# Performance work log

Hardware: AMD Instinct MI355X
Metric: run time of the kernel (lower is better)

The kernel has to match this reference:

```python
import jax, jax.numpy as jnp
import numpy as np

DEPTH = 2
TWO_PI = 6.283185307179586


def _apply_ry(state, theta, axis):
    """Apply RY(theta) on qubit at `axis` of state [N,2,2,2,2]. theta: [N] or scalar."""
    half = theta * 0.5
    a0 = jnp.take(state, 0, axis=axis)  # [N,2,2,2]
    a1 = jnp.take(state, 1, axis=axis)
    c = jnp.reshape(jnp.cos(half), (-1,) + (1,) * (a0.ndim - 1))
    s = jnp.reshape(jnp.sin(half), (-1,) + (1,) * (a0.ndim - 1))
    return jnp.stack([c * a0 - s * a1, s * a0 + c * a1], axis=axis)


def _apply_cnot(state, c_axis, t_axis):
    a0 = jnp.take(state, 0, axis=c_axis)  # control=0: unchanged
    a1 = jnp.take(state, 1, axis=c_axis)  # control=1: flip target
    t_ax = t_axis - (1 if t_axis > c_axis else 0)
    a1 = jnp.flip(a1, axis=t_ax)
    return jnp.stack([a0, a1], axis=c_axis)


def _simulate(patches, weights):
    """patches: [N,4] angles. Returns <Z_i> for i=0..3, shape [N,4]. All gates real."""
    N = patches.shape[0]
    state = jnp.zeros((N, 2, 2, 2, 2), dtype=patches.dtype)
    state = state.at[:, 0, 0, 0, 0].set(1.0)
    for w in range(4):  # data encoding
        state = _apply_ry(state, patches[:, w], axis=w + 1)
    for d in range(DEPTH):  # variational layers
        for w in range(4):
            state = _apply_ry(state, weights[d, w], axis=w + 1)
        for c, t in ((0, 1), (1, 2), (2, 3)):
            state = _apply_cnot(state, c + 1, t + 1)
    probs = state * state
    zs = []
    for w in range(4):
        p0 = jnp.take(probs, 0, axis=w + 1).sum(axis=(1, 2, 3))
        p1 = jnp.take(probs, 1, axis=w + 1).sum(axis=(1, 2, 3))
        zs.append(p0 - p1)
    return jnp.stack(zs, axis=-1)  # [N,4]


def setup_inputs() -> dict:
    key = jax.random.key(0)
    k1, k2, k3, k4 = jax.random.split(key, 4)
    B = 8192
    x = jax.random.uniform(k1, (B, 1, 28, 28), dtype=jnp.float32)
    weights = jax.random.uniform(k2, (DEPTH, 4), dtype=jnp.float32) * TWO_PI
    W = jax.random.normal(k3, (10, 4 * 14 * 14), dtype=jnp.float32) * 0.02
    b = jax.random.normal(k4, (10,), dtype=jnp.float32) * 0.02
    return {"x": x, "weights": weights, "W": W, "b": b}


def reference(x, weights, W, b):
    B = x.shape[0]
    # Extract non-overlapping 2x2 patches in row-major (i,j) order;
    # within a patch, order is [(i,j),(i,j+1),(i+1,j),(i+1,j+1)] matching x[:,:,i:i+2,j:j+2].view(B,4)
    p = x.reshape(B, 14, 2, 14, 2).transpose(0, 1, 3, 2, 4).reshape(B, 196, 4)
    feats = _simulate(p.reshape(B * 196, 4), weights).reshape(B, 196 * 4)
    logits = feats @ W.T + b
    return jax.nn.log_softmax(logits, axis=-1)
```

## Files before the change

kernel.cpp:

```cpp
#include <hip/hip_runtime.h>
#include <math.h>

#define INV2PI 0.15915494309189535f

__device__ __forceinline__ float rfl(float v) {
    return __int_as_float(__builtin_amdgcn_readfirstlane(__float_as_int(v)));
}

__global__ __launch_bounds__(256) void quanv_w4_kernel(
    const float* __restrict__ x,
    const float* __restrict__ wts,
    const float* __restrict__ W,
    const float* __restrict__ bias,
    float* __restrict__ out,
    int B)
{
    const int lane  = threadIdx.x & 63;
    const int img0  = (blockIdx.x * 4 + (threadIdx.x >> 6)) * 4;
    if (img0 >= B) return;

    float w0r[4], cw1[4], sw1[4];
#pragma unroll
    for (int q = 0; q < 4; ++q) {
        w0r[q] = rfl(wts[q] * INV2PI);
        float r = wts[4 + q] * INV2PI;
        r -= floorf(r);
        cw1[q] = __builtin_amdgcn_cosf(r);
        sw1[q] = __builtin_amdgcn_sinf(r);
    }
    const float cc  = cw1[0]*cw1[1], cs = cw1[0]*sw1[1];
    const float sc  = sw1[0]*cw1[1], ss = sw1[0]*sw1[1];
    const float ccc = cc*cw1[2], ccs = cc*sw1[2], csc = cs*cw1[2], css = cs*sw1[2];
    const float scc = sc*cw1[2], ssc = ss*cw1[2], sss = ss*sw1[2];
    const float K0 = rfl(cw1[0]),       K1 = rfl(-sw1[0]);
    const float K2 = rfl(cc),           K3 = rfl(-cs),          K4 = rfl(ss);
    const float K5 = rfl(ccc),          K6 = rfl(-ccs),         K7 = rfl(css);
    const float K8 = rfl(-scc),         K9 = rfl(-sss);
    const float L1 = rfl(ccc*cw1[3]),   L2 = rfl(-ccc*sw1[3]);
    const float L3 = rfl(ccs*sw1[3]),   L4 = rfl(-csc*cw1[3]);
    const float L5 = rfl(-css*sw1[3]),  L6 = rfl(scc*sw1[3]);
    const float L7 = rfl(ssc*cw1[3]),   L8 = rfl(sss*sw1[3]);

    float acc[4][10];
#pragma unroll
    for (int im = 0; im < 4; ++im)
#pragma unroll
        for (int cl = 0; cl < 10; ++cl) acc[im][cl] = 0.f;

#pragma unroll
    for (int i = 0; i < 4; ++i) {
        const int p = i * 64 + lane;
        if (p < 196) {
            const int pi = p / 14, pj = p - pi * 14;
            const int xoff = pi * 56 + pj * 2;

            float4 wv[10];
#pragma unroll
            for (int cl = 0; cl < 10; ++cl)
                wv[cl] = *(const float4*)(W + cl * 784 + p * 4);

#pragma unroll
            for (int im = 0; im < 4; ++im) {
                if (img0 + im < B) {
                    const float* xp = x + (size_t)(img0 + im) * 784 + xoff;
                    const float2 t0 = *(const float2*)xp;
                    const float2 t1 = *(const float2*)(xp + 28);

                    float r;
                    r = fmaf(t0.x, INV2PI, w0r[0]); r -= floorf(r);
                    const float a  = __builtin_amdgcn_sinf(r), A  = __builtin_amdgcn_cosf(r);
                    r = fmaf(t0.y, INV2PI, w0r[1]); r -= floorf(r);
                    const float b  = __builtin_amdgcn_sinf(r), Bv = __builtin_amdgcn_cosf(r);
                    r = fmaf(t1.x, INV2PI, w0r[2]); r -= floorf(r);
                    const float c  = __builtin_amdgcn_sinf(r), C  = __builtin_amdgcn_cosf(r);
                    r = fmaf(t1.y, INV2PI, w0r[3]); r -= floorf(r);
                    const float d  = __builtin_amdgcn_sinf(r), D  = __builtin_amdgcn_cosf(r);

                    const float ab=a*b, bc=b*c, ac=a*c, cd=c*d, bd=b*d, ad=a*d;
                    const float AC=A*C, Ab=A*b, Bc=Bv*c, BD=Bv*D, cD=c*D, Cd=C*d;

                    const float z0 = fmaf(K0, A,  K1*ab);
                    const float z1 = fmaf(K2, Bv, fmaf(K3, A*bc, K4*ac));
                    const float z2 = fmaf(K5, AC, fmaf(K6, Bv*cd,
                                     fmaf(K7, A*bd, fmaf(K8, ab*C, K9*ad))));
                    const float z3 = fmaf(L1, BD, fmaf(L2, AC*d, fmaf(L3, Bc,
                                     fmaf(L4, Ab*cD, fmaf(L5, Ab, fmaf(L6, ab*Cd,
                                     fmaf(L7, ac*D, L8*a)))))));

#pragma unroll
                    for (int cl = 0; cl < 10; ++cl)
                        acc[im][cl] = fmaf(z0, wv[cl].x, fmaf(z1, wv[cl].y,
                                      fmaf(z2, wv[cl].z, fmaf(z3, wv[cl].w, acc[im][cl]))));
                }
            }
        }
    }

#pragma unroll
    for (int im = 0; im < 4; ++im) {
        if (img0 + im < B) {
            float lg[10];
#pragma unroll
            for (int cl = 0; cl < 10; ++cl) {
                float v = acc[im][cl];
                v += __shfl_xor(v, 1, 64);
                v += __shfl_xor(v, 2, 64);
                v += __shfl_xor(v, 4, 64);
                v += __shfl_xor(v, 8, 64);
                v += __shfl_xor(v, 16, 64);
                v += __shfl_xor(v, 32, 64);
                lg[cl] = v + bias[cl];
            }
            float m = lg[0];
#pragma unroll
            for (int cl = 1; cl < 10; ++cl) m = fmaxf(m, lg[cl]);
            float s = 0.f;
#pragma unroll
            for (int cl = 0; cl < 10; ++cl) s += __expf(lg[cl] - m);
            const float lse = m + __logf(s);

            if (lane == 0) {
                float* op = out + (size_t)(img0 + im) * 10;
                *(float2*)(op + 0) = make_float2(lg[0] - lse, lg[1] - lse);
                *(float2*)(op + 2) = make_float2(lg[2] - lse, lg[3] - lse);
                *(float2*)(op + 4) = make_float2(lg[4] - lse, lg[5] - lse);
                *(float2*)(op + 6) = make_float2(lg[6] - lse, lg[7] - lse);
                *(float2*)(op + 8) = make_float2(lg[8] - lse, lg[9] - lse);
            }
        }
    }
}

extern "C" void kernel_launch(void* const* d_in, const int* in_sizes, int n_in,
                              void* d_out, int out_size, void* d_ws, size_t ws_size,
                              hipStream_t stream) {
    const float* x    = (const float*)d_in[0];
    const float* wts  = (const float*)d_in[1];
    const float* W    = (const float*)d_in[2];
    const float* bias = (const float*)d_in[3];
    float* out        = (float*)d_out;

    const int B = in_sizes[0] / 784;
    const int blocks = (B + 15) / 16;
    quanv_w4_kernel<<<blocks, 256, 0, stream>>>(x, wts, W, bias, out, B);
}
```

Measured before the change: 20.29 us.

## Split patch range across wave pairs and reduce partial logits via shared memory

Each group of four images is now handled by two waves, each covering 98 of the 196 patches. This removes the idle lanes of the old 4x64 patch loop and doubles the number of blocks. Partial sums are reduced with three shuffle steps, then combined across lanes and waves in shared memory, followed by a small softmax stage and a coalesced output write. The W loads are moved inside the class loop to lower register pressure, and launch bounds now request occupancy. The cost is extra block barriers and shared-memory traffic.

```diff
diff --git a/kernel.cpp b/kernel.cpp
--- a/kernel.cpp
+++ b/kernel.cpp
@@ -7,7 +7,7 @@
     return __int_as_float(__builtin_amdgcn_readfirstlane(__float_as_int(v)));
 }
 
-__global__ __launch_bounds__(256) void quanv_w4_kernel(
+__global__ __launch_bounds__(256, 4) void quanv_ks_kernel(
     const float* __restrict__ x,
     const float* __restrict__ wts,
     const float* __restrict__ W,
@@ -15,9 +15,15 @@
     float* __restrict__ out,
     int B)
 {
-    const int lane  = threadIdx.x & 63;
-    const int img0  = (blockIdx.x * 4 + (threadIdx.x >> 6)) * 4;
-    if (img0 >= B) return;
+    __shared__ float part[4][8][40];
+    __shared__ float logits[8][10];
+    __shared__ float lsev[8];
+
+    const int tid   = threadIdx.x;
+    const int wave  = tid >> 6, lane = tid & 63;
+    const int group = wave >> 1;
+    const int half  = wave & 1;
+    const int imgb  = blockIdx.x * 8 + group * 4;
 
     float w0r[4], cw1[4], sw1[4];
 #pragma unroll
@@ -48,21 +54,18 @@
         for (int cl = 0; cl < 10; ++cl) acc[im][cl] = 0.f;
 
 #pragma unroll
-    for (int i = 0; i < 4; ++i) {
-        const int p = i * 64 + lane;
-        if (p < 196) {
+    for (int it = 0; it < 2; ++it) {
+        if (it == 0 || lane < 34) {
+            const int p  = half * 98 + it * 64 + lane;
             const int pi = p / 14, pj = p - pi * 14;
             const int xoff = pi * 56 + pj * 2;
 
-            float4 wv[10];
-#pragma unroll
-            for (int cl = 0; cl < 10; ++cl)
-                wv[cl] = *(const float4*)(W + cl * 784 + p * 4);
-
+            float z[4][4];
 #pragma unroll
             for (int im = 0; im < 4; ++im) {
-                if (img0 + im < B) {
-                    const float* xp = x + (size_t)(img0 + im) * 784 + xoff;
+                const int img = imgb + im;
+                if (img < B) {
+                    const float* xp = x + (size_t)img * 784 + xoff;
                     const float2 t0 = *(const float2*)xp;
                     const float2 t1 = *(const float2*)(xp + 28);
 
@@ -79,55 +82,71 @@
                     const float ab=a*b, bc=b*c, ac=a*c, cd=c*d, bd=b*d, ad=a*d;
                     const float AC=A*C, Ab=A*b, Bc=Bv*c, BD=Bv*D, cD=c*D, Cd=C*d;
 
-                    const float z0 = fmaf(K0, A,  K1*ab);
-                    const float z1 = fmaf(K2, Bv, fmaf(K3, A*bc, K4*ac));
-                    const float z2 = fmaf(K5, AC, fmaf(K6, Bv*cd,
-                                     fmaf(K7, A*bd, fmaf(K8, ab*C, K9*ad))));
-                    const float z3 = fmaf(L1, BD, fmaf(L2, AC*d, fmaf(L3, Bc,
-                                     fmaf(L4, Ab*cD, fmaf(L5, Ab, fmaf(L6, ab*Cd,
-                                     fmaf(L7, ac*D, L8*a)))))));
+                    z[im][0] = fmaf(K0, A,  K1*ab);
+                    z[im][1] = fmaf(K2, Bv, fmaf(K3, A*bc, K4*ac));
+                    z[im][2] = fmaf(K5, AC, fmaf(K6, Bv*cd,
+                               fmaf(K7, A*bd, fmaf(K8, ab*C, K9*ad))));
+                    z[im][3] = fmaf(L1, BD, fmaf(L2, AC*d, fmaf(L3, Bc,
+                               fmaf(L4, Ab*cD, fmaf(L5, Ab, fmaf(L6, ab*Cd,
+                               fmaf(L7, ac*D, L8*a)))))));
+                } else {
+                    z[im][0] = z[im][1] = z[im][2] = z[im][3] = 0.f;
+                }
+            }
 
 #pragma unroll
-                    for (int cl = 0; cl < 10; ++cl)
-                        acc[im][cl] = fmaf(z0, wv[cl].x, fmaf(z1, wv[cl].y,
-                                      fmaf(z2, wv[cl].z, fmaf(z3, wv[cl].w, acc[im][cl]))));
-                }
+            for (int cl = 0; cl < 10; ++cl) {
+                const float4 wv = *(const float4*)(W + cl * 784 + p * 4);
+#pragma unroll
+                for (int im = 0; im < 4; ++im)
+                    acc[im][cl] = fmaf(z[im][0], wv.x, fmaf(z[im][1], wv.y,
+                                  fmaf(z[im][2], wv.z, fmaf(z[im][3], wv.w, acc[im][cl]))));
             }
         }
     }
 
 #pragma unroll
-    for (int im = 0; im < 4; ++im) {
-        if (img0 + im < B) {
-            float lg[10];
+    for (int im = 0; im < 4; ++im)
 #pragma unroll
-            for (int cl = 0; cl < 10; ++cl) {
-                float v = acc[im][cl];
-                v += __shfl_xor(v, 1, 64);
-                v += __shfl_xor(v, 2, 64);
-                v += __shfl_xor(v, 4, 64);
-                v += __shfl_xor(v, 8, 64);
-                v += __shfl_xor(v, 16, 64);
-                v += __shfl_xor(v, 32, 64);
-                lg[cl] = v + bias[cl];
-            }
-            float m = lg[0];
+        for (int cl = 0; cl < 10; ++cl) {
+            float v = acc[im][cl];
+            v += __shfl_xor(v, 1, 64);
+            v += __shfl_xor(v, 2, 64);
+            v += __shfl_xor(v, 4, 64);
+            if ((lane & 7) == 0) part[wave][lane >> 3][im * 10 + cl] = v;
+        }
+    __syncthreads();
+
+    if (tid < 80) {
+        const int g  = tid / 40;
+        const int vv = tid - g * 40;
+        const int im = vv / 10, cl = vv - im * 10;
+        float s = 0.f;
 #pragma unroll
-            for (int cl = 1; cl < 10; ++cl) m = fmaxf(m, lg[cl]);
+        for (int l = 0; l < 8; ++l)
+            s += part[2 * g][l][vv] + part[2 * g + 1][l][vv];
+        logits[g * 4 + im][cl] = s + bias[cl];
+    }
+    __syncthreads();
+
+    if (tid < 8) {
+        if (blockIdx.x * 8 + tid < B) {
+            float m = logits[tid][0];
+#pragma unroll
+            for (int cl = 1; cl < 10; ++cl) m = fmaxf(m, logits[tid][cl]);
             float s = 0.f;
 #pragma unroll
-            for (int cl = 0; cl < 10; ++cl) s += __expf(lg[cl] - m);
-            const float lse = m + __logf(s);
+            for (int cl = 0; cl < 10; ++cl) s += __expf(logits[tid][cl] - m);
+            lsev[tid] = m + __logf(s);
+        }
+    }
+    __syncthreads();
 
-            if (lane == 0) {
-                float* op = out + (size_t)(img0 + im) * 10;
-                *(float2*)(op + 0) = make_float2(lg[0] - lse, lg[1] - lse);
-                *(float2*)(op + 2) = make_float2(lg[2] - lse, lg[3] - lse);
-                *(float2*)(op + 4) = make_float2(lg[4] - lse, lg[5] - lse);
-                *(float2*)(op + 6) = make_float2(lg[6] - lse, lg[7] - lse);
-                *(float2*)(op + 8) = make_float2(lg[8] - lse, lg[9] - lse);
-            }
-        }
+    if (tid < 80) {
+        const int imloc = tid / 10, cl = tid - (tid / 10) * 10;
+        const int img = blockIdx.x * 8 + imloc;
+        if (img < B)
+            out[(size_t)img * 10 + cl] = logits[imloc][cl] - lsev[imloc];
     }
 }
 
@@ -141,6 +160,6 @@
     float* out        = (float*)d_out;
 
     const int B = in_sizes[0] / 784;
-    const int blocks = (B + 15) / 16;
-    quanv_w4_kernel<<<blocks, 256, 0, stream>>>(x, wts, W, bias, out, B);
+    const int blocks = (B + 7) / 8;
+    quanv_ks_kernel<<<blocks, 256, 0, stream>>>(x, wts, W, bias, out, B);
 }
```

Result: faster. 18.73 us (-7.7%).

## Split fused kernel into feature kernel writing bf16 features and separate GEMM kernel

Applied to the files above, without the earlier changes.

Replaces the single fused kernel with two launches. The first computes the four qubit expectation values per patch, one thread per patch, and stores them as bf16 in the workspace. The second reads those bf16 features and does the 784x10 matvec plus log-softmax. This aims for better occupancy in the trig-heavy stage. In exchange it adds an extra launch, a round trip of about 13 MB through global memory, and bf16 rounding of the features. The GEMM kernel also drops the per-image bounds check on its loads.

```diff
diff --git a/kernel.cpp b/kernel.cpp
--- a/kernel.cpp
+++ b/kernel.cpp
@@ -1,4 +1,5 @@
 #include <hip/hip_runtime.h>
+#include <hip/hip_bf16.h>
 #include <math.h>
 
 #define INV2PI 0.15915494309189535f
@@ -7,19 +8,10 @@
     return __int_as_float(__builtin_amdgcn_readfirstlane(__float_as_int(v)));
 }
 
-__global__ __launch_bounds__(256) void quanv_w4_kernel(
-    const float* __restrict__ x,
-    const float* __restrict__ wts,
-    const float* __restrict__ W,
-    const float* __restrict__ bias,
-    float* __restrict__ out,
-    int B)
-{
-    const int lane  = threadIdx.x & 63;
-    const int img0  = (blockIdx.x * 4 + (threadIdx.x >> 6)) * 4;
-    if (img0 >= B) return;
+struct KL { float K0,K1,K2,K3,K4,K5,K6,K7,K8,K9,L1,L2,L3,L4,L5,L6,L7,L8; };
 
-    float w0r[4], cw1[4], sw1[4];
+__device__ __forceinline__ KL make_kl(const float* wts, float* w0r) {
+    float cw1[4], sw1[4];
 #pragma unroll
     for (int q = 0; q < 4; ++q) {
         w0r[q] = rfl(wts[q] * INV2PI);
@@ -32,14 +24,80 @@
     const float sc  = sw1[0]*cw1[1], ss = sw1[0]*sw1[1];
     const float ccc = cc*cw1[2], ccs = cc*sw1[2], csc = cs*cw1[2], css = cs*sw1[2];
     const float scc = sc*cw1[2], ssc = ss*cw1[2], sss = ss*sw1[2];
-    const float K0 = rfl(cw1[0]),       K1 = rfl(-sw1[0]);
-    const float K2 = rfl(cc),           K3 = rfl(-cs),          K4 = rfl(ss);
-    const float K5 = rfl(ccc),          K6 = rfl(-ccs),         K7 = rfl(css);
-    const float K8 = rfl(-scc),         K9 = rfl(-sss);
-    const float L1 = rfl(ccc*cw1[3]),   L2 = rfl(-ccc*sw1[3]);
-    const float L3 = rfl(ccs*sw1[3]),   L4 = rfl(-csc*cw1[3]);
-    const float L5 = rfl(-css*sw1[3]),  L6 = rfl(scc*sw1[3]);
-    const float L7 = rfl(ssc*cw1[3]),   L8 = rfl(sss*sw1[3]);
+    KL k;
+    k.K0 = rfl(cw1[0]);      k.K1 = rfl(-sw1[0]);
+    k.K2 = rfl(cc);          k.K3 = rfl(-cs);         k.K4 = rfl(ss);
+    k.K5 = rfl(ccc);         k.K6 = rfl(-ccs);        k.K7 = rfl(css);
+    k.K8 = rfl(-scc);        k.K9 = rfl(-sss);
+    k.L1 = rfl(ccc*cw1[3]);  k.L2 = rfl(-ccc*sw1[3]);
+    k.L3 = rfl(ccs*sw1[3]);  k.L4 = rfl(-csc*cw1[3]);
+    k.L5 = rfl(-css*sw1[3]); k.L6 = rfl(scc*sw1[3]);
+    k.L7 = rfl(ssc*cw1[3]);  k.L8 = rfl(sss*sw1[3]);
+    return k;
+}
+
+__global__ __launch_bounds__(256) void quanv_feat_kernel(
+    const float* __restrict__ x,
+    const float* __restrict__ wts,
+    __hip_bfloat16* __restrict__ feats,
+    int NP)
+{
+    const int pid = blockIdx.x * 256 + threadIdx.x;
+    if (pid >= NP) return;
+
+    float w0r[4];
+    const KL k = make_kl(wts, w0r);
+
+    const int img = pid / 196;
+    const int pl  = pid - img * 196;
+    const int pi  = pl / 14, pj = pl - pi * 14;
+    const float* xp = x + (size_t)img * 784 + pi * 56 + pj * 2;
+    const float2 t0 = *(const float2*)xp;
+    const float2 t1 = *(const float2*)(xp + 28);
+
+    float r;
+    r = fmaf(t0.x, INV2PI, w0r[0]); r -= floorf(r);
+    const float a  = __builtin_amdgcn_sinf(r), A  = __builtin_amdgcn_cosf(r);
+    r = fmaf(t0.y, INV2PI, w0r[1]); r -= floorf(r);
+    const float b  = __builtin_amdgcn_sinf(r), Bv = __builtin_amdgcn_cosf(r);
+    r = fmaf(t1.x, INV2PI, w0r[2]); r -= floorf(r);
+    const float c  = __builtin_amdgcn_sinf(r), C  = __builtin_amdgcn_cosf(r);
+    r = fmaf(t1.y, INV2PI, w0r[3]); r -= floorf(r);
+    const float d  = __builtin_amdgcn_sinf(r), D  = __builtin_amdgcn_cosf(r);
+
+    const float ab=a*b, bc=b*c, ac=a*c, cd=c*d, bd=b*d, ad=a*d;
+    const float AC=A*C, Ab=A*b, Bc=Bv*c, BD=Bv*D, cD=c*D, Cd=C*d;
+
+    const float z0 = fmaf(k.K0, A,  k.K1*ab);
+    const float z1 = fmaf(k.K2, Bv, fmaf(k.K3, A*bc, k.K4*ac));
+    const float z2 = fmaf(k.K5, AC, fmaf(k.K6, Bv*cd,
+                     fmaf(k.K7, A*bd, fmaf(k.K8, ab*C, k.K9*ad))));
+    const float z3 = fmaf(k.L1, BD, fmaf(k.L2, AC*d, fmaf(k.L3, Bc,
+                     fmaf(k.L4, Ab*cD, fmaf(k.L5, Ab, fmaf(k.L6, ab*Cd,
+                     fmaf(k.L7, ac*D, k.L8*a)))))));
+
+    union { ushort4 u; __hip_bfloat16 h[4]; } pk;
+    pk.h[0] = __float2bfloat16(z0);
+    pk.h[1] = __float2bfloat16(z1);
+    pk.h[2] = __float2bfloat16(z2);
+    pk.h[3] = __float2bfloat16(z3);
+    *(ushort4*)(feats + (size_t)pid * 4) = pk.u;
+}
+
+__device__ __forceinline__ float bf2f(unsigned short u) {
+    return __uint_as_float(((unsigned int)u) << 16);
+}
+
+__global__ __launch_bounds__(256) void quanv_gemm_kernel(
+    const __hip_bfloat16* __restrict__ feats,
+    const float* __restrict__ W,
+    const float* __restrict__ bias,
+    float* __restrict__ out,
+    int B)
+{
+    const int lane  = threadIdx.x & 63;
+    const int img0  = (blockIdx.x * 4 + (threadIdx.x >> 6)) * 4;
+    if (img0 >= B) return;
 
     float acc[4][10];
 #pragma unroll
@@ -51,47 +109,18 @@
     for (int i = 0; i < 4; ++i) {
         const int p = i * 64 + lane;
         if (p < 196) {
-            const int pi = p / 14, pj = p - pi * 14;
-            const int xoff = pi * 56 + pj * 2;
-
-            float4 wv[10];
+            ushort4 f[4];
 #pragma unroll
-            for (int cl = 0; cl < 10; ++cl)
-                wv[cl] = *(const float4*)(W + cl * 784 + p * 4);
-
+            for (int im = 0; im < 4; ++im)
+                f[im] = *(const ushort4*)(feats + ((size_t)(img0 + im) * 196 + p) * 4);
 #pragma unroll
-            for (int im = 0; im < 4; ++im) {
-                if (img0 + im < B) {
-                    const float* xp = x + (size_t)(img0 + im) * 784 + xoff;
-                    const float2 t0 = *(const float2*)xp;
-                    const float2 t1 = *(const float2*)(xp + 28);
-
-                    float r;
-                    r = fmaf(t0.x, INV2PI, w0r[0]); r -= floorf(r);
-                    const float a  = __builtin_amdgcn_sinf(r), A  = __builtin_amdgcn_cosf(r);
-                    r = fmaf(t0.y, INV2PI, w0r[1]); r -= floorf(r);
-                    const float b  = __builtin_amdgcn_sinf(r), Bv = __builtin_amdgcn_cosf(r);
-                    r = fmaf(t1.x, INV2PI, w0r[2]); r -= floorf(r);
-                    const float c  = __builtin_amdgcn_sinf(r), C  = __builtin_amdgcn_cosf(r);
-                    r = fmaf(t1.y, INV2PI, w0r[3]); r -= floorf(r);
-                    const float d  = __builtin_amdgcn_sinf(r), D  = __builtin_amdgcn_cosf(r);
-
-                    const float ab=a*b, bc=b*c, ac=a*c, cd=c*d, bd=b*d, ad=a*d;
-                    const float AC=A*C, Ab=A*b, Bc=Bv*c, BD=Bv*D, cD=c*D, Cd=C*d;
-
-                    const float z0 = fmaf(K0, A,  K1*ab);
-                    const float z1 = fmaf(K2, Bv, fmaf(K3, A*bc, K4*ac));
-                    const float z2 = fmaf(K5, AC, fmaf(K6, Bv*cd,
-                                     fmaf(K7, A*bd, fmaf(K8, ab*C, K9*ad))));
-                    const float z3 = fmaf(L1, BD, fmaf(L2, AC*d, fmaf(L3, Bc,
-                                     fmaf(L4, Ab*cD, fmaf(L5, Ab, fmaf(L6, ab*Cd,
-                                     fmaf(L7, ac*D, L8*a)))))));
-
+            for (int cl = 0; cl < 10; ++cl) {
+                const float4 wv = *(const float4*)(W + cl * 784 + p * 4);
 #pragma unroll
-                    for (int cl = 0; cl < 10; ++cl)
-                        acc[im][cl] = fmaf(z0, wv[cl].x, fmaf(z1, wv[cl].y,
-                                      fmaf(z2, wv[cl].z, fmaf(z3, wv[cl].w, acc[im][cl]))));
-                }
+                for (int im = 0; im < 4; ++im)
+                    acc[im][cl] = fmaf(bf2f(f[im].x), wv.x, fmaf(bf2f(f[im].y), wv.y,
+                                  fmaf(bf2f(f[im].z), wv.z, fmaf(bf2f(f[im].w), wv.w,
+                                  acc[im][cl]))));
             }
         }
     }
@@ -118,7 +147,6 @@
 #pragma unroll
             for (int cl = 0; cl < 10; ++cl) s += __expf(lg[cl] - m);
             const float lse = m + __logf(s);
-
             if (lane == 0) {
                 float* op = out + (size_t)(img0 + im) * 10;
                 *(float2*)(op + 0) = make_float2(lg[0] - lse, lg[1] - lse);
@@ -139,8 +167,11 @@
     const float* W    = (const float*)d_in[2];
     const float* bias = (const float*)d_in[3];
     float* out        = (float*)d_out;
+    __hip_bfloat16* feats = (__hip_bfloat16*)d_ws;
 
-    const int B = in_sizes[0] / 784;
-    const int blocks = (B + 15) / 16;
-    quanv_w4_kernel<<<blocks, 256, 0, stream>>>(x, wts, W, bias, out, B);
+    const int B  = in_sizes[0] / 784;
+    const int NP = B * 196;
+
+    quanv_feat_kernel<<<(NP + 255) / 256, 256, 0, stream>>>(x, wts, feats, NP);
+    quanv_gemm_kernel<<<(B + 15) / 16, 256, 0, stream>>>(feats, W, bias, out, B);
 }
```

After: 26.58 us. 31.0% more time.
